# Performance work log

Hardware: AMD Instinct MI355X
Metric: run time of the kernel (lower is better)

The kernel has to match this reference:

```python
import jax, jax.numpy as jnp
import numpy as np

N_USER, N_VIDEO, N_PUB, N_TAG = 200000, 100000, 20000, 5000
EMB = 128
HALF = EMB // 2
LAYER_NUM = 3


def setup_inputs() -> dict:
    key = jax.random.key(0)
    ks = jax.random.split(key, 20)
    inp = {
        "user_emb": jax.random.normal(ks[0], (N_USER, EMB), jnp.float32),
        "video_emb": jax.random.normal(ks[1], (N_VIDEO, EMB), jnp.float32),
        "publisher_emb": jax.random.normal(ks[2], (N_PUB, EMB), jnp.float32),
        "tag_emb": jax.random.normal(ks[3], (N_TAG, EMB), jnp.float32),
    }
    # (name, E, n_src, n_dst)
    rels = [
        ("uv", 1500000, N_USER, N_VIDEO),
        ("vu", 1500000, N_VIDEO, N_USER),
        ("up", 800000, N_USER, N_PUB),
        ("pu", 800000, N_PUB, N_USER),
        ("vt", 800000, N_VIDEO, N_TAG),
        ("tv", 800000, N_TAG, N_VIDEO),
        ("pt", 400000, N_PUB, N_TAG),
        ("tp", 400000, N_TAG, N_PUB),
    ]
    for i, (name, E, ns, nd) in enumerate(rels):
        inp[name + "_src"] = jax.random.randint(ks[4 + 2 * i], (E,), 0, ns, jnp.int32)
        inp[name + "_dst"] = jax.random.randint(ks[5 + 2 * i], (E,), 0, nd, jnp.int32)
    return inp


def _seg_mean(feat, src, dst, num_dst):
    # copy_u + mean: gather half-dim src features, segment-mean onto dst.
    msg = feat[src]                                             # [E, HALF]
    s = jax.ops.segment_sum(msg, dst, num_segments=num_dst)     # [num_dst, HALF]
    deg = jax.ops.segment_sum(jnp.ones_like(dst, dtype=feat.dtype), dst,
                              num_segments=num_dst)
    return s / jnp.maximum(deg, 1.0)[:, None]  # zero-in-degree nodes -> 0 (DGL behavior)


def reference(user_emb, video_emb, publisher_emb, tag_emb,
              uv_src, uv_dst, vu_src, vu_dst,
              up_src, up_dst, pu_src, pu_dst,
              vt_src, vt_dst, tv_src, tv_dst,
              pt_src, pt_dst, tp_src, tp_dst):

    def layer(u, v, p, t):
        # user dst: [vu, pu]; video dst: [uv, tv]; publisher dst: [up, tp]; tag dst: [vt, pt]
        vu = _seg_mean(v[:, :HALF], vu_src, vu_dst, N_USER)
        pu = _seg_mean(p[:, :HALF], pu_src, pu_dst, N_USER)
        uv = _seg_mean(u[:, :HALF], uv_src, uv_dst, N_VIDEO)
        tv = _seg_mean(t[:, :HALF], tv_src, tv_dst, N_VIDEO)
        up = _seg_mean(u[:, HALF:], up_src, up_dst, N_PUB)
        tp = _seg_mean(t[:, HALF:], tp_src, tp_dst, N_PUB)
        vt = _seg_mean(v[:, HALF:], vt_src, vt_dst, N_TAG)
        pt = _seg_mean(p[:, HALF:], pt_src, pt_dst, N_TAG)
        return (jnp.concatenate([vu, pu], axis=1),
                jnp.concatenate([uv, tv], axis=1),
                jnp.concatenate([up, tp], axis=1),
                jnp.concatenate([vt, pt], axis=1))

    pu_, pv_, pp_, pt_ = user_emb, video_emb, publisher_emb, tag_emb
    u, v, p, t = user_emb, video_emb, publisher_emb, tag_emb
    for i in range(LAYER_NUM):
        u, v, p, t = layer(u, v, p, t)
        w = 1.0 / (i + 2)
        pu_ = pu_ + u * w
        pv_ = pv_ + v * w
        pp_ = pp_ + p * w
        pt_ = pt_ + t * w
    return (pu_, pv_, pp_, pt_)
```

## Files before the change

kernel.cpp:

```cpp
#include <hip/hip_runtime.h>
#include <hip/hip_bf16.h>
#include <stdint.h>

#define EMB 128
#define CAP 12288

static constexpr int N_USER = 200000, N_VIDEO = 100000, N_PUB = 20000, N_TAG = 5000;
static constexpr int ROW_U = 0, ROW_V = 200000, ROW_P = 300000, ROW_T = 320000;
static constexpr int ROWS = 325000;
static constexpr int TOTAL_E = 7000000;
static constexpr int TOTAL_GROUPS = 650000;
static constexpr int TILE = 4096;

__device__ inline unsigned bf16_rne(float f) {
  unsigned u = __float_as_uint(f);
  return (u + 0x7fffu + ((u >> 16) & 1u)) >> 16;
}
__device__ inline unsigned pack_bf16x2(float lo, float hi) {
  return bf16_rne(lo) | (bf16_rne(hi) << 16);
}

struct SortDesc {
  int tcum[9];
  int bcum[9];
  int gcum[8];
  int E[8];
  int n_dst[8];
  int wshift[8];
  const int* esrc[8];
  const int* edst[8];
};

struct AggrDesc {
  int cum[9];
  int src_base[8];
  int src_col[8];
  int dst_base[8];
  int dst_col[8];
  const float* demb[8];
};

__global__ __launch_bounds__(256) void part_kernel(SortDesc d, unsigned* __restrict__ pairs,
                                                   int* __restrict__ cursors) {
  __shared__ int cnt[256];
  __shared__ int lcur[256];
  int blk = blockIdx.x;
  int r = 0;
#pragma unroll
  for (int k = 1; k < 8; ++k) if (blk >= d.tcum[k]) r = k;
  int base = (blk - d.tcum[r]) * TILE;
  int n = min(TILE, d.E[r] - base);
  const int* __restrict__ esrc = d.esrc[r];
  const int* __restrict__ edst = d.edst[r];
  int tid = threadIdx.x;
  int B = d.bcum[r + 1] - d.bcum[r];
  int sh = d.wshift[r];
  int msk = (1 << sh) - 1;
  int bb = d.bcum[r];
  if (tid < B) cnt[tid] = 0;
  __syncthreads();
  for (int i = tid; i < n; i += 256)
    atomicAdd(&cnt[edst[base + i] >> sh], 1);
  __syncthreads();
  if (tid < B) {
    int c = cnt[tid];
    lcur[tid] = c ? atomicAdd(&cursors[bb + tid], c) : 0;
  }
  __syncthreads();
  for (int i = tid; i < n; i += 256) {
    int dv = edst[base + i];
    int sv = esrc[base + i];
    int b = dv >> sh;
    int pos = atomicAdd(&lcur[b], 1);
    if (pos < CAP)
      pairs[(size_t)(bb + b) * CAP + pos] = ((unsigned)(dv & msk) << 18) | (unsigned)sv;
  }
}

__global__ __launch_bounds__(256) void bases_kernel(const int* __restrict__ cursors,
                                                    int* __restrict__ bases, int NB) {
  __shared__ int wsums[4];
  int tid = threadIdx.x;
  int L = (NB + 255) / 256;
  int lo = min(tid * L, NB), hi = min(lo + L, NB);
  int s = 0;
  for (int i = lo; i < hi; ++i) s += cursors[i];
  int lane = tid & 63, wv = tid >> 6;
  int v = s;
#pragma unroll
  for (int dd = 1; dd < 64; dd <<= 1) {
    int t = __shfl_up(v, dd);
    if (lane >= dd) v += t;
  }
  if (lane == 63) wsums[wv] = v;
  __syncthreads();
  if (tid == 0) {
    int run = 0;
#pragma unroll
    for (int k = 0; k < 4; ++k) { int t = wsums[k]; wsums[k] = run; run += t; }
  }
  __syncthreads();
  int run = wsums[wv] + (v - s);
  for (int i = lo; i < hi; ++i) { int c = cursors[i]; bases[i] = run; run += c; }
}

__global__ __launch_bounds__(256) void build_kernel(SortDesc d, const unsigned* __restrict__ pairs,
                                                    const int* __restrict__ cursors,
                                                    const int* __restrict__ bases,
                                                    int* __restrict__ sorted,
                                                    int* __restrict__ Beg, int* __restrict__ Deg) {
  __shared__ int cnt[1024];
  __shared__ int stage[CAP];
  __shared__ int wsums[4];
  int bucket = blockIdx.x;
  int r = 0;
#pragma unroll
  for (int k = 1; k < 8; ++k) if (bucket >= d.bcum[k]) r = k;
  int bl = bucket - d.bcum[r];
  int sh = d.wshift[r];
  int first = bl << sh;
  int Wa = min(1 << sh, d.n_dst[r] - first);
  int tid = threadIdx.x;
  int n_b = min(cursors[bucket], CAP);
  int gbase = bases[bucket];
  const unsigned* __restrict__ bp = pairs + (size_t)bucket * CAP;

  for (int i = tid; i < 1024; i += 256) cnt[i] = 0;
  __syncthreads();
  for (int i = tid; i < n_b; i += 256)
    atomicAdd(&cnt[bp[i] >> 18], 1);
  __syncthreads();

  int t4 = tid * 4;
  int c0 = cnt[t4], c1 = cnt[t4 + 1], c2 = cnt[t4 + 2], c3 = cnt[t4 + 3];
  int s = c0 + c1 + c2 + c3;
  int lane = tid & 63, wv = tid >> 6;
  int v = s;
#pragma unroll
  for (int dd = 1; dd < 64; dd <<= 1) {
    int t = __shfl_up(v, dd);
    if (lane >= dd) v += t;
  }
  if (lane == 63) wsums[wv] = v;
  __syncthreads();
  if (tid == 0) {
    int run = 0;
#pragma unroll
    for (int k = 0; k < 4; ++k) { int t = wsums[k]; wsums[k] = run; run += t; }
  }
  __syncthreads();
  int ex = wsums[wv] + (v - s);
  int o0 = ex, o1 = ex + c0, o2 = o1 + c1, o3 = o2 + c2;
  cnt[t4] = o0; cnt[t4 + 1] = o1; cnt[t4 + 2] = o2; cnt[t4 + 3] = o3;
  int g0 = d.gcum[r] + first + t4;
  if (t4 + 0 < Wa) { Beg[g0 + 0] = gbase + o0; Deg[g0 + 0] = c0; }
  if (t4 + 1 < Wa) { Beg[g0 + 1] = gbase + o1; Deg[g0 + 1] = c1; }
  if (t4 + 2 < Wa) { Beg[g0 + 2] = gbase + o2; Deg[g0 + 2] = c2; }
  if (t4 + 3 < Wa) { Beg[g0 + 3] = gbase + o3; Deg[g0 + 3] = c3; }
  __syncthreads();

  for (int i = tid; i < n_b; i += 256) {
    unsigned pr = bp[i];
    int pos = atomicAdd(&cnt[pr >> 18], 1);
    stage[pos] = (int)(pr & 0x3FFFFu);
  }
  __syncthreads();
  for (int i = tid; i < n_b; i += 256)
    sorted[gbase + i] = stage[i];
}

__global__ void convert_kernel(const float* __restrict__ u, const float* __restrict__ v,
                               const float* __restrict__ p, const float* __restrict__ t,
                               uint16_t* __restrict__ feat) {
  int idx = blockIdx.x * blockDim.x + threadIdx.x;
  const int total4 = ROWS * EMB / 4;
  if (idx >= total4) return;
  int flat = idx * 4;
  int row = flat >> 7;
  int col = flat & 127;
  const float* s;
  if (row < ROW_V)      s = u + (size_t)row * EMB + col;
  else if (row < ROW_P) s = v + (size_t)(row - ROW_V) * EMB + col;
  else if (row < ROW_T) s = p + (size_t)(row - ROW_P) * EMB + col;
  else                  s = t + (size_t)(row - ROW_T) * EMB + col;
  float4 f = *(const float4*)s;
  uint2 o;
  o.x = pack_bf16x2(f.x, f.y);
  o.y = pack_bf16x2(f.z, f.w);
  *(uint2*)(feat + flat) = o;
}

#define ACC(q) \
  a0 += __uint_as_float((q).x << 16); a1 += __uint_as_float((q).x & 0xffff0000u); \
  a2 += __uint_as_float((q).y << 16); a3 += __uint_as_float((q).y & 0xffff0000u); \
  a4 += __uint_as_float((q).z << 16); a5 += __uint_as_float((q).z & 0xffff0000u); \
  a6 += __uint_as_float((q).w << 16); a7 += __uint_as_float((q).w & 0xffff0000u);

__global__ __launch_bounds__(256) void aggr_kernel(AggrDesc d, const uint16_t* __restrict__ prev,
                                                   uint16_t* __restrict__ next,
                                                   float* __restrict__ out, int mode,
                                                   const int* __restrict__ sorted,
                                                   const int* __restrict__ Beg,
                                                   const int* __restrict__ Deg) {
  int g = blockIdx.x * 32 + (threadIdx.x >> 3);
  if (g >= TOTAL_GROUPS) return;
  int lane = threadIdx.x & 7;
  int r = 0;
#pragma unroll
  for (int k = 1; k < 8; ++k) if (g >= d.cum[k]) r = k;
  int n = g - d.cum[r];
  int beg = Beg[g], dg = Deg[g];
  float recip = 1.0f / (float)(dg > 0 ? dg : 1);
  const uint16_t* sbase = prev + (size_t)d.src_base[r] * EMB + d.src_col[r] + lane * 8;
  float a0 = 0.f, a1 = 0.f, a2 = 0.f, a3 = 0.f, a4 = 0.f, a5 = 0.f, a6 = 0.f, a7 = 0.f;
  int e = beg, end = beg + dg;
  for (; e + 4 <= end; e += 4) {
    int s0 = sorted[e], s1 = sorted[e + 1], s2 = sorted[e + 2], s3 = sorted[e + 3];
    uint4 q0 = *(const uint4*)(sbase + (size_t)s0 * EMB);
    uint4 q1 = *(const uint4*)(sbase + (size_t)s1 * EMB);
    uint4 q2 = *(const uint4*)(sbase + (size_t)s2 * EMB);
    uint4 q3 = *(const uint4*)(sbase + (size_t)s3 * EMB);
    ACC(q0); ACC(q1); ACC(q2); ACC(q3);
  }
  for (; e < end; ++e) {
    int s0 = sorted[e];
    uint4 q = *(const uint4*)(sbase + (size_t)s0 * EMB);
    ACC(q);
  }
  a0 *= recip; a1 *= recip; a2 *= recip; a3 *= recip;
  a4 *= recip; a5 *= recip; a6 *= recip; a7 *= recip;

  int col = d.dst_col[r] + lane * 8;
  size_t dpos = (size_t)(d.dst_base[r] + n) * EMB + col;

  if (mode == 0) {
    uint4 ov;
    ov.x = pack_bf16x2(a0, a1);
    ov.y = pack_bf16x2(a2, a3);
    ov.z = pack_bf16x2(a4, a5);
    ov.w = pack_bf16x2(a6, a7);
    *(uint4*)(next + dpos) = ov;
    return;
  }

  uint4 q1 = *(const uint4*)(next + dpos);
  uint4 q2 = *(const uint4*)(prev + dpos);
  const float* de = d.demb[r] + (size_t)n * EMB + col;
  float4 v0 = *(const float4*)de;
  float4 v1 = *((const float4*)de + 1);
  const float w1 = 0.5f, w2 = 1.0f / 3.0f, w3 = 0.25f;
  v0.x += w1 * __uint_as_float(q1.x << 16)        + w2 * __uint_as_float(q2.x << 16)        + w3 * a0;
  v0.y += w1 * __uint_as_float(q1.x & 0xffff0000u) + w2 * __uint_as_float(q2.x & 0xffff0000u) + w3 * a1;
  v0.z += w1 * __uint_as_float(q1.y << 16)        + w2 * __uint_as_float(q2.y << 16)        + w3 * a2;
  v0.w += w1 * __uint_as_float(q1.y & 0xffff0000u) + w2 * __uint_as_float(q2.y & 0xffff0000u) + w3 * a3;
  v1.x += w1 * __uint_as_float(q1.z << 16)        + w2 * __uint_as_float(q2.z << 16)        + w3 * a4;
  v1.y += w1 * __uint_as_float(q1.z & 0xffff0000u) + w2 * __uint_as_float(q2.z & 0xffff0000u) + w3 * a5;
  v1.z += w1 * __uint_as_float(q1.w << 16)        + w2 * __uint_as_float(q2.w << 16)        + w3 * a6;
  v1.w += w1 * __uint_as_float(q1.w & 0xffff0000u) + w2 * __uint_as_float(q2.w & 0xffff0000u) + w3 * a7;
  *(float4*)(out + dpos) = v0;
  *((float4*)(out + dpos) + 1) = v1;
}

extern "C" void kernel_launch(void* const* d_in, const int* in_sizes, int n_in,
                              void* d_out, int out_size, void* d_ws, size_t ws_size,
                              hipStream_t stream) {
  const float* emb_u = (const float*)d_in[0];
  const float* emb_v = (const float*)d_in[1];
  const float* emb_p = (const float*)d_in[2];
  const float* emb_t = (const float*)d_in[3];

  struct RelInfo { int si, di, E, n_dst, src_base, src_col, dst_base, dst_col, wshift; };
  const RelInfo rels[8] = {
    {12, 13,  800000, N_TAG,   ROW_V, 64, ROW_T,  0,  5},
    {16, 17,  400000, N_TAG,   ROW_P, 64, ROW_T, 64,  5},
    { 8,  9,  800000, N_PUB,   ROW_U, 64, ROW_P,  0,  7},
    {18, 19,  400000, N_PUB,   ROW_T, 64, ROW_P, 64,  7},
    { 4,  5, 1500000, N_VIDEO, ROW_U,  0, ROW_V,  0,  9},
    {14, 15,  800000, N_VIDEO, ROW_T,  0, ROW_V, 64,  9},
    { 6,  7, 1500000, N_USER,  ROW_V,  0, ROW_U,  0, 10},
    {10, 11,  800000, N_USER,  ROW_P,  0, ROW_U, 64, 10},
  };
  const float* dembs[8] = {emb_t, emb_t, emb_p, emb_p, emb_v, emb_v, emb_u, emb_u};

  char* ws = (char*)d_ws;
  size_t cursor = 0;
  auto take = [&](size_t bytes) -> char* {
    char* p = ws + cursor;
    cursor = (cursor + bytes + 255) & ~(size_t)255;
    return p;
  };
  uint16_t* featA = (uint16_t*)take((size_t)ROWS * EMB * 2);
  uint16_t* featB = (uint16_t*)take((size_t)ROWS * EMB * 2);
  int* sorted = (int*)take((size_t)TOTAL_E * 4);
  int* Beg    = (int*)take((size_t)TOTAL_GROUPS * 4);
  int* Deg    = (int*)take((size_t)TOTAL_GROUPS * 4);
  unsigned* pairs = (unsigned*)d_ws;

  SortDesc sd;
  AggrDesc ad;
  int tacc = 0, bacc = 0, gacc = 0;
  for (int r = 0; r < 8; ++r) {
    int n_dst = rels[r].n_dst;
    sd.tcum[r] = tacc; tacc += (rels[r].E + TILE - 1) / TILE;
    sd.bcum[r] = bacc; bacc += (n_dst + (1 << rels[r].wshift) - 1) >> rels[r].wshift;
    sd.gcum[r] = gacc;
    sd.E[r] = rels[r].E;
    sd.n_dst[r] = n_dst;
    sd.wshift[r] = rels[r].wshift;
    sd.esrc[r] = (const int*)d_in[rels[r].si];
    sd.edst[r] = (const int*)d_in[rels[r].di];

    ad.cum[r] = gacc;
    ad.src_base[r] = rels[r].src_base;
    ad.src_col[r] = rels[r].src_col;
    ad.dst_base[r] = rels[r].dst_base;
    ad.dst_col[r] = rels[r].dst_col;
    ad.demb[r] = dembs[r];
    gacc += n_dst;
  }
  sd.tcum[8] = tacc;
  sd.bcum[8] = bacc;
  ad.cum[8] = gacc;

  int* cursors = (int*)take((size_t)bacc * 4);
  int* bases   = (int*)take((size_t)bacc * 4);

  hipMemsetAsync(cursors, 0, (size_t)bacc * 4, stream);
  part_kernel<<<tacc, 256, 0, stream>>>(sd, pairs, cursors);
  bases_kernel<<<1, 256, 0, stream>>>(cursors, bases, bacc);
  build_kernel<<<bacc, 256, 0, stream>>>(sd, pairs, cursors, bases, sorted, Beg, Deg);

  convert_kernel<<<(ROWS * EMB / 4 + 255) / 256, 256, 0, stream>>>(emb_u, emb_v, emb_p, emb_t, featA);

  float* out = (float*)d_out;
  const int aggr_blocks = (TOTAL_GROUPS + 31) / 32;
  aggr_kernel<<<aggr_blocks, 256, 0, stream>>>(ad, featA, featB, out, 0, sorted, Beg, Deg);
  aggr_kernel<<<aggr_blocks, 256, 0, stream>>>(ad, featB, featA, out, 0, sorted, Beg, Deg);
  aggr_kernel<<<aggr_blocks, 256, 0, stream>>>(ad, featA, featB, out, 1, sorted, Beg, Deg);
}
```

Baseline: 639.5 us.

## Cooperatively load edge indices via shuffles, widen convert stores, enlarge partition tile

In the aggregation kernel, each 8-lane group now loads 8 sorted source indices with one coalesced read and broadcasts them with shuffles. It then issues 8 independent row gathers before accumulating, where before each lane read 4 indices itself per step. The convert kernel handles 8 floats per thread with one 16-byte store. The partition TILE constant doubles, which changes how many edges each sort block processes. The goal is fewer redundant index loads and more memory-level parallelism, at the cost of higher register pressure from the q[8] buffer.

Result: faster. 618.8 us (-3.2%).

```diff
diff --git a/kernel.cpp b/kernel.cpp
--- a/kernel.cpp
+++ b/kernel.cpp
@@ -10,7 +10,7 @@
 static constexpr int ROWS = 325000;
 static constexpr int TOTAL_E = 7000000;
 static constexpr int TOTAL_GROUPS = 650000;
-static constexpr int TILE = 4096;
+static constexpr int TILE = 8192;
 
 __device__ inline unsigned bf16_rne(float f) {
   unsigned u = __float_as_uint(f);
@@ -173,9 +173,9 @@
                                const float* __restrict__ p, const float* __restrict__ t,
                                uint16_t* __restrict__ feat) {
   int idx = blockIdx.x * blockDim.x + threadIdx.x;
-  const int total4 = ROWS * EMB / 4;
-  if (idx >= total4) return;
-  int flat = idx * 4;
+  const int total8 = ROWS * EMB / 8;
+  if (idx >= total8) return;
+  int flat = idx * 8;
   int row = flat >> 7;
   int col = flat & 127;
   const float* s;
@@ -183,11 +183,14 @@
   else if (row < ROW_P) s = v + (size_t)(row - ROW_V) * EMB + col;
   else if (row < ROW_T) s = p + (size_t)(row - ROW_P) * EMB + col;
   else                  s = t + (size_t)(row - ROW_T) * EMB + col;
-  float4 f = *(const float4*)s;
-  uint2 o;
-  o.x = pack_bf16x2(f.x, f.y);
-  o.y = pack_bf16x2(f.z, f.w);
-  *(uint2*)(feat + flat) = o;
+  float4 f0 = *(const float4*)s;
+  float4 f1 = *((const float4*)s + 1);
+  uint4 o;
+  o.x = pack_bf16x2(f0.x, f0.y);
+  o.y = pack_bf16x2(f0.z, f0.w);
+  o.z = pack_bf16x2(f1.x, f1.y);
+  o.w = pack_bf16x2(f1.z, f1.w);
+  *(uint4*)(feat + flat) = o;
 }
 
 #define ACC(q) \
@@ -214,18 +217,33 @@
   const uint16_t* sbase = prev + (size_t)d.src_base[r] * EMB + d.src_col[r] + lane * 8;
   float a0 = 0.f, a1 = 0.f, a2 = 0.f, a3 = 0.f, a4 = 0.f, a5 = 0.f, a6 = 0.f, a7 = 0.f;
   int e = beg, end = beg + dg;
-  for (; e + 4 <= end; e += 4) {
-    int s0 = sorted[e], s1 = sorted[e + 1], s2 = sorted[e + 2], s3 = sorted[e + 3];
-    uint4 q0 = *(const uint4*)(sbase + (size_t)s0 * EMB);
-    uint4 q1 = *(const uint4*)(sbase + (size_t)s1 * EMB);
-    uint4 q2 = *(const uint4*)(sbase + (size_t)s2 * EMB);
-    uint4 q3 = *(const uint4*)(sbase + (size_t)s3 * EMB);
-    ACC(q0); ACC(q1); ACC(q2); ACC(q3);
-  }
-  for (; e < end; ++e) {
-    int s0 = sorted[e];
-    uint4 q = *(const uint4*)(sbase + (size_t)s0 * EMB);
-    ACC(q);
+  while (e + 8 <= end) {
+    int myi = sorted[e + lane];
+    uint4 q[8];
+#pragma unroll
+    for (int j = 0; j < 8; ++j) {
+      int sj = __shfl(myi, j, 8);
+      q[j] = *(const uint4*)(sbase + (size_t)sj * EMB);
+    }
+#pragma unroll
+    for (int j = 0; j < 8; ++j) { ACC(q[j]); }
+    e += 8;
+  }
+  int rem = end - e;
+  if (rem > 0) {
+    int myi = sorted[e + (lane < rem ? lane : 0)];
+    uint4 q[7];
+#pragma unroll
+    for (int j = 0; j < 7; ++j) {
+      if (j < rem) {
+        int sj = __shfl(myi, j, 8);
+        q[j] = *(const uint4*)(sbase + (size_t)sj * EMB);
+      }
+    }
+#pragma unroll
+    for (int j = 0; j < 7; ++j) {
+      if (j < rem) { ACC(q[j]); }
+    }
   }
   a0 *= recip; a1 *= recip; a2 *= recip; a3 *= recip;
   a4 *= recip; a5 *= recip; a6 *= recip; a7 *= recip;
@@ -249,13 +267,13 @@
   float4 v0 = *(const float4*)de;
   float4 v1 = *((const float4*)de + 1);
   const float w1 = 0.5f, w2 = 1.0f / 3.0f, w3 = 0.25f;
-  v0.x += w1 * __uint_as_float(q1.x << 16)        + w2 * __uint_as_float(q2.x << 16)        + w3 * a0;
+  v0.x += w1 * __uint_as_float(q1.x << 16)         + w2 * __uint_as_float(q2.x << 16)         + w3 * a0;
   v0.y += w1 * __uint_as_float(q1.x & 0xffff0000u) + w2 * __uint_as_float(q2.x & 0xffff0000u) + w3 * a1;
-  v0.z += w1 * __uint_as_float(q1.y << 16)        + w2 * __uint_as_float(q2.y << 16)        + w3 * a2;
+  v0.z += w1 * __uint_as_float(q1.y << 16)         + w2 * __uint_as_float(q2.y << 16)         + w3 * a2;
   v0.w += w1 * __uint_as_float(q1.y & 0xffff0000u) + w2 * __uint_as_float(q2.y & 0xffff0000u) + w3 * a3;
-  v1.x += w1 * __uint_as_float(q1.z << 16)        + w2 * __uint_as_float(q2.z << 16)        + w3 * a4;
+  v1.x += w1 * __uint_as_float(q1.z << 16)         + w2 * __uint_as_float(q2.z << 16)         + w3 * a4;
   v1.y += w1 * __uint_as_float(q1.z & 0xffff0000u) + w2 * __uint_as_float(q2.z & 0xffff0000u) + w3 * a5;
-  v1.z += w1 * __uint_as_float(q1.w << 16)        + w2 * __uint_as_float(q2.w << 16)        + w3 * a6;
+  v1.z += w1 * __uint_as_float(q1.w << 16)         + w2 * __uint_as_float(q2.w << 16)         + w3 * a6;
   v1.w += w1 * __uint_as_float(q1.w & 0xffff0000u) + w2 * __uint_as_float(q2.w & 0xffff0000u) + w3 * a7;
   *(float4*)(out + dpos) = v0;
   *((float4*)(out + dpos) + 1) = v1;
@@ -330,7 +348,7 @@
   bases_kernel<<<1, 256, 0, stream>>>(cursors, bases, bacc);
   build_kernel<<<bacc, 256, 0, stream>>>(sd, pairs, cursors, bases, sorted, Beg, Deg);
 
-  convert_kernel<<<(ROWS * EMB / 4 + 255) / 256, 256, 0, stream>>>(emb_u, emb_v, emb_p, emb_t, featA);
+  convert_kernel<<<(ROWS * EMB / 8 + 255) / 256, 256, 0, stream>>>(emb_u, emb_v, emb_p, emb_t, featA);
 
   float* out = (float*)d_out;
   const int aggr_blocks = (TOTAL_GROUPS + 31) / 32;
```
